# Performance work log

Measured on AMD Instinct MI355X. Metric: run time of the kernel, lower is better.

The kernel has to match this reference:

```python
import jax, jax.numpy as jnp
import numpy as np

B, C, H, W = 4096, 2, 64, 64
D = 1.0 / (H - 1)  # grid spacing d0 = d1
CLAMP_MIN = -27.6310211159


def fd1_last(f, d):
    # 2nd-order accurate first derivative along last axis, non-periodic.
    c = (f[..., 2:] - f[..., :-2]) / (2.0 * d)
    lo = (-3.0 * f[..., 0:1] + 4.0 * f[..., 1:2] - f[..., 2:3]) / (2.0 * d)
    hi = (3.0 * f[..., -1:] - 4.0 * f[..., -2:-1] + f[..., -3:-2]) / (2.0 * d)
    return jnp.concatenate([lo, c, hi], axis=-1)


def fd2_last(f, d):
    # 2nd-order accurate second derivative along last axis, non-periodic.
    d2 = d * d
    c = (f[..., 2:] - 2.0 * f[..., 1:-1] + f[..., :-2]) / d2
    lo = (2.0 * f[..., 0:1] - 5.0 * f[..., 1:2] + 4.0 * f[..., 2:3] - f[..., 3:4]) / d2
    hi = (2.0 * f[..., -1:] - 5.0 * f[..., -2:-1] + 4.0 * f[..., -3:-2] - f[..., -4:-3]) / d2
    return jnp.concatenate([lo, c, hi], axis=-1)


def fd_axis(f, d, axis, order):
    fn = fd1_last if order == 1 else fd2_last
    if axis == -1 or axis == f.ndim - 1:
        return fn(f, d)
    g = jnp.swapaxes(f, axis, -1)
    return jnp.swapaxes(fn(g, d), axis, -1)


def darcy_source(h, w, r=10.0, w_frac=0.125):
    ww = int(round(w_frac * h))
    f = np.zeros((h, w), dtype=np.float32)
    f[:ww, :ww] = r
    f[-ww:, -ww:] = -r
    return jnp.asarray(f)


def compute_residual(x0):
    # x0: (B, 2, H, W) with channel 0 = pressure p, channel 1 = permeability K
    p, perm = x0[:, 0], x0[:, 1]
    p_d0 = fd_axis(p, D, -2, 1)
    p_d1 = fd_axis(p, D, -1, 1)
    p_d00 = fd_axis(p, D, -2, 2)
    p_d11 = fd_axis(p, D, -1, 2)
    perm_d0 = fd_axis(perm, D, -2, 1)
    perm_d1 = fd_axis(perm, D, -1, 1)

    f_s = darcy_source(H, W)  # (H, W)
    # div(-K grad p) - f  (only diagonal of velocity jacobian is populated)
    eq0 = (-perm * p_d00 - perm_d0 * p_d0) + (-perm * p_d11 - perm_d1 * p_d1) - f_s  # (B,H,W)

    # Neumann boundary residuals on grad p (channel 0 = d/d0, channel 1 = d/d1)
    bc = jnp.zeros((x0.shape[0], 2, H, W), dtype=x0.dtype)
    bc = bc.at[:, 0, 0, :].set(-p_d0[:, 0, :])
    bc = bc.at[:, 0, -1, :].set(p_d0[:, -1, :])
    bc = bc.at[:, 1, :, 0].set(p_d1[:, :, 0])
    bc = bc.at[:, 1, :, -1].set(-p_d1[:, :, -1])

    # b c x y -> b (x y) c  layout, then concat eq0 as an extra channel
    eq0_flat = eq0.reshape(eq0.shape[0], H * W, 1)
    bc_flat = jnp.transpose(bc, (0, 2, 3, 1)).reshape(bc.shape[0], H * W, 2)
    residual = jnp.concatenate([eq0_flat, bc_flat], axis=-1)  # (B, HW, 3)
    return residual.mean(axis=(1, 2))  # (B,)


def darcy_loss(model_out, target, x0_hat, var):
    data_loss = jnp.mean((model_out - target) ** 2)
    r = compute_residual(x0_hat)  # (B,)
    ll = -0.5 * (r ** 2) / var  # gaussian log-likelihood of 0 under N(r, var)
    ll = jnp.maximum(ll, CLAMP_MIN)
    residual_loss = jnp.mean(-ll)
    c_residual = 1.0
    return data_loss + c_residual * residual_loss


def setup_inputs() -> dict:
    key = jax.random.key(0)
    k1, k2, k3, k4 = jax.random.split(key, 4)
    return {
        "model_out": jax.random.normal(k1, (B, C, H, W), dtype=jnp.float32),
        "target": jax.random.normal(k2, (B, C, H, W), dtype=jnp.float32),
        "x0_hat": jax.random.normal(k3, (B, C, H, W), dtype=jnp.float32),
        "var": jax.random.uniform(k4, (B,), dtype=jnp.float32, minval=0.5, maxval=1.5),
    }


def reference(model_out, target, x0_hat, var):
    return darcy_loss(model_out, target, x0_hat, var)
```

## Files before the change

kernel.cpp:

```cpp
#include <hip/hip_runtime.h>


#define NB 4096
#define HW 4096
#define CHW 8192

__device__ __forceinline__ void hderiv2(float v, int j, float& d1, float& d11) {
    constexpr float INV2D = 31.5f, INVD2 = 3969.0f;
    float vm = __shfl(v, (j + 63) & 63);
    float vp = __shfl(v, (j + 1) & 63);
    float v2 = __shfl(v, (j == 0) ? 2 : 61);
    float v3 = __shfl(v, (j == 0) ? 3 : 60);
    d1  = (vp - vm) * INV2D;
    d11 = (vp - 2.0f * v + vm) * INVD2;
    if (j == 0)  { d1 = (-3.0f * v + 4.0f * vp - v2) * INV2D;
                   d11 = (2.0f * v - 5.0f * vp + 4.0f * v2 - v3) * INVD2; }
    if (j == 63) { d1 = ( 3.0f * v - 4.0f * vm + v2) * INV2D;
                   d11 = (2.0f * v - 5.0f * vm + 4.0f * v2 - v3) * INVD2; }
}

__device__ __forceinline__ float hderiv1(float v, int j) {
    constexpr float INV2D = 31.5f;
    float vm = __shfl(v, (j + 63) & 63);
    float vp = __shfl(v, (j + 1) & 63);
    float v2 = __shfl(v, (j == 0) ? 2 : 61);
    float d = (vp - vm) * INV2D;
    if (j == 0)  d = (-3.0f * v + 4.0f * vp - v2) * INV2D;
    if (j == 63) d = ( 3.0f * v - 4.0f * vm + v2) * INV2D;
    return d;
}

__global__ __launch_bounds__(256, 8) void darcy_wave_kernel(
    const float* __restrict__ mo, const float* __restrict__ tg,
    const float* __restrict__ x0, const float* __restrict__ var,
    float* __restrict__ ws_res, float* __restrict__ ws_data)
{
    constexpr float INV2D = 31.5f;
    constexpr float INVD2 = 3969.0f;
    constexpr float CLAMP = 27.6310211159f;

    const int wave = threadIdx.x >> 6;
    const int j    = threadIdx.x & 63;
    const int b    = blockIdx.x * 4 + wave;

    const float*  pb = x0 + (size_t)b * CHW;
    const float*  qb = pb + HW;
    const float4* m4 = (const float4*)(mo + (size_t)b * CHW);
    const float4* g4 = (const float4*)(tg + (size_t)b * CHW);

    float rsum = 0.0f, dsum = 0.0f;

    float pm = pb[j], pc = pb[64 + j], pp = pb[128 + j], pn = pb[192 + j];
    float qm = qb[j], qc = qb[64 + j], qp = qb[128 + j], qn = qb[192 + j];

    {
        float pd1, pd11;
        hderiv2(pm, j, pd1, pd11);
        float qd1 = hderiv1(qm, j);
        float pd0  = (-3.0f * pm + 4.0f * pc - pp) * INV2D;
        float pd00 = (2.0f * pm - 5.0f * pc + 4.0f * pp - pn) * INVD2;
        float qd0  = (-3.0f * qm + 4.0f * qc - qp) * INV2D;
        rsum += -qm * (pd00 + pd11) - qd0 * pd0 - qd1 * pd1 - pd0;
        rsum += (j == 0) ? pd1 : 0.0f;
        rsum -= (j == 63) ? pd1 : 0.0f;
    }

    float s_p60 = 0.0f, s_p61 = 0.0f, s_q61 = 0.0f;

    #pragma unroll 2
    for (int i = 1; i <= 62; ++i) {
        float pn2 = 0.0f, qn2 = 0.0f;
        if (i <= 60) {
            pn2 = pb[((i + 3) << 6) + j];
            qn2 = qb[((i + 3) << 6) + j];
        }
        if (i <= 32) {
            const int k = (i - 1) << 6;
            float4 a = m4[j + k];
            float4 c = g4[j + k];
            float e0 = a.x - c.x, e1 = a.y - c.y, e2 = a.z - c.z, e3 = a.w - c.w;
            dsum += e0 * e0 + e1 * e1 + e2 * e2 + e3 * e3;
        }

        float pd1, pd11;
        hderiv2(pc, j, pd1, pd11);
        float qd1 = hderiv1(qc, j);
        float pd0  = (pp - pm) * INV2D;
        float pd00 = (pp - 2.0f * pc + pm) * INVD2;
        float qd0  = (qp - qm) * INV2D;
        rsum += -qc * (pd00 + pd11) - qd0 * pd0 - qd1 * pd1;
        rsum += (j == 0) ? pd1 : 0.0f;
        rsum -= (j == 63) ? pd1 : 0.0f;

        if (i == 61) s_p60 = pm;
        if (i == 62) { s_p61 = pm; s_q61 = qm; }

        pm = pc; pc = pp; pp = pn; pn = pn2;
        qm = qc; qc = qp; qp = qn; qn = qn2;
    }

    {
        float pd1, pd11;
        hderiv2(pc, j, pd1, pd11);
        float qd1 = hderiv1(qc, j);
        float pd0  = (3.0f * pc - 4.0f * pm + s_p61) * INV2D;
        float pd00 = (2.0f * pc - 5.0f * pm + 4.0f * s_p61 - s_p60) * INVD2;
        float qd0  = (3.0f * qc - 4.0f * qm + s_q61) * INV2D;
        rsum += -qc * (pd00 + pd11) - qd0 * pd0 - qd1 * pd1 + pd0;
        rsum += (j == 0) ? pd1 : 0.0f;
        rsum -= (j == 63) ? pd1 : 0.0f;
    }

    #pragma unroll
    for (int off = 32; off > 0; off >>= 1) {
        rsum += __shfl_down(rsum, off);
        dsum += __shfl_down(dsum, off);
    }
    if (j == 0) {
        const float r = rsum * (1.0f / (64.0f * 64.0f * 3.0f));
        float res = 0.5f * r * r / var[b];
        ws_res[b]  = fminf(res, CLAMP);
        ws_data[b] = dsum;
    }
}

__global__ __launch_bounds__(256) void darcy_final_kernel(
    const float* __restrict__ ws_res, const float* __restrict__ ws_data,
    float* __restrict__ out)
{
    const int t = threadIdx.x;
    double rs = 0.0, ds = 0.0;
    for (int i = t; i < NB; i += 256) {
        rs += (double)ws_res[i];
        ds += (double)ws_data[i];
    }
    #pragma unroll
    for (int off = 32; off > 0; off >>= 1) {
        rs += __shfl_down(rs, off);
        ds += __shfl_down(ds, off);
    }
    __shared__ double red[8];
    const int wid = t >> 6, lane = t & 63;
    if (lane == 0) { red[wid] = rs; red[4 + wid] = ds; }
    __syncthreads();
    if (t == 0) {
        const double R  = red[0] + red[1] + red[2] + red[3];
        const double Dd = red[4] + red[5] + red[6] + red[7];
        out[0] = (float)(Dd / ((double)NB * (double)CHW) + R / (double)NB);
    }
}

extern "C" void kernel_launch(void* const* d_in, const int* in_sizes, int n_in,
                              void* d_out, int out_size, void* d_ws, size_t ws_size,
                              hipStream_t stream) {
    const float* mo  = (const float*)d_in[0];
    const float* tg  = (const float*)d_in[1];
    const float* x0  = (const float*)d_in[2];
    const float* var = (const float*)d_in[3];
    float* out = (float*)d_out;

    float* ws_res  = (float*)d_ws;
    float* ws_data = ws_res + NB;

    darcy_wave_kernel<<<NB / 4, 256, 0, stream>>>(mo, tg, x0, var, ws_res, ws_data);
    darcy_final_kernel<<<1, 256, 0, stream>>>(ws_res, ws_data, out);
}
```

Measured before the change: 84.90 us.

## Split each batch row-sweep across two waves to double parallelism

Each batch element is now handled by two waves, one sweeping rows 0-31 and the other rows 32-63, with the data-loss float4 loads divided between them. Partial sums for each half go to the workspace, and the final kernel combines the halves before applying the variance scaling and clamp. The aim is more waves in flight and a shorter serial sweep per wave, which helps hide memory latency. The cost is some extra halo row loads, twice as many blocks, and a final kernel that reads twice the workspace plus the var array.

```diff
diff --git a/kernel.cpp b/kernel.cpp
--- a/kernel.cpp
+++ b/kernel.cpp
@@ -32,16 +32,15 @@
 
 __global__ __launch_bounds__(256, 8) void darcy_wave_kernel(
     const float* __restrict__ mo, const float* __restrict__ tg,
-    const float* __restrict__ x0, const float* __restrict__ var,
-    float* __restrict__ ws_res, float* __restrict__ ws_data)
+    const float* __restrict__ x0, float* __restrict__ ws_r, float* __restrict__ ws_d)
 {
     constexpr float INV2D = 31.5f;
     constexpr float INVD2 = 3969.0f;
-    constexpr float CLAMP = 27.6310211159f;
 
     const int wave = threadIdx.x >> 6;
     const int j    = threadIdx.x & 63;
-    const int b    = blockIdx.x * 4 + wave;
+    const int half = wave & 1;
+    const int b    = blockIdx.x * 2 + (wave >> 1);
 
     const float*  pb = x0 + (size_t)b * CHW;
     const float*  qb = pb + HW;
@@ -50,65 +49,103 @@
 
     float rsum = 0.0f, dsum = 0.0f;
 
-    float pm = pb[j], pc = pb[64 + j], pp = pb[128 + j], pn = pb[192 + j];
-    float qm = qb[j], qc = qb[64 + j], qp = qb[128 + j], qn = qb[192 + j];
-
-    {
-        float pd1, pd11;
-        hderiv2(pm, j, pd1, pd11);
-        float qd1 = hderiv1(qm, j);
-        float pd0  = (-3.0f * pm + 4.0f * pc - pp) * INV2D;
-        float pd00 = (2.0f * pm - 5.0f * pc + 4.0f * pp - pn) * INVD2;
-        float qd0  = (-3.0f * qm + 4.0f * qc - qp) * INV2D;
-        rsum += -qm * (pd00 + pd11) - qd0 * pd0 - qd1 * pd1 - pd0;
-        rsum += (j == 0) ? pd1 : 0.0f;
-        rsum -= (j == 63) ? pd1 : 0.0f;
-    }
-
-    float s_p60 = 0.0f, s_p61 = 0.0f, s_q61 = 0.0f;
-
-    #pragma unroll 2
-    for (int i = 1; i <= 62; ++i) {
-        float pn2 = 0.0f, qn2 = 0.0f;
-        if (i <= 60) {
-            pn2 = pb[((i + 3) << 6) + j];
-            qn2 = qb[((i + 3) << 6) + j];
-        }
-        if (i <= 32) {
-            const int k = (i - 1) << 6;
-            float4 a = m4[j + k];
-            float4 c = g4[j + k];
+    if (half == 0) {
+        float pm = pb[j], pc = pb[64 + j], pp = pb[128 + j], pn = pb[192 + j];
+        float qm = qb[j], qc = qb[64 + j], qp = qb[128 + j], qn = qb[192 + j];
+
+        {
+            float4 a = m4[j], c = g4[j];
             float e0 = a.x - c.x, e1 = a.y - c.y, e2 = a.z - c.z, e3 = a.w - c.w;
             dsum += e0 * e0 + e1 * e1 + e2 * e2 + e3 * e3;
-        }
-
-        float pd1, pd11;
-        hderiv2(pc, j, pd1, pd11);
-        float qd1 = hderiv1(qc, j);
-        float pd0  = (pp - pm) * INV2D;
-        float pd00 = (pp - 2.0f * pc + pm) * INVD2;
-        float qd0  = (qp - qm) * INV2D;
-        rsum += -qc * (pd00 + pd11) - qd0 * pd0 - qd1 * pd1;
-        rsum += (j == 0) ? pd1 : 0.0f;
-        rsum -= (j == 63) ? pd1 : 0.0f;
-
-        if (i == 61) s_p60 = pm;
-        if (i == 62) { s_p61 = pm; s_q61 = qm; }
-
-        pm = pc; pc = pp; pp = pn; pn = pn2;
-        qm = qc; qc = qp; qp = qn; qn = qn2;
-    }
-
-    {
-        float pd1, pd11;
-        hderiv2(pc, j, pd1, pd11);
-        float qd1 = hderiv1(qc, j);
-        float pd0  = (3.0f * pc - 4.0f * pm + s_p61) * INV2D;
-        float pd00 = (2.0f * pc - 5.0f * pm + 4.0f * s_p61 - s_p60) * INVD2;
-        float qd0  = (3.0f * qc - 4.0f * qm + s_q61) * INV2D;
-        rsum += -qc * (pd00 + pd11) - qd0 * pd0 - qd1 * pd1 + pd0;
-        rsum += (j == 0) ? pd1 : 0.0f;
-        rsum -= (j == 63) ? pd1 : 0.0f;
+
+            float pd1, pd11;
+            hderiv2(pm, j, pd1, pd11);
+            float qd1 = hderiv1(qm, j);
+            float pd0  = (-3.0f * pm + 4.0f * pc - pp) * INV2D;
+            float pd00 = (2.0f * pm - 5.0f * pc + 4.0f * pp - pn) * INVD2;
+            float qd0  = (-3.0f * qm + 4.0f * qc - qp) * INV2D;
+            rsum += -qm * (pd00 + pd11) - qd0 * pd0 - qd1 * pd1 - pd0;
+            rsum += (j == 0) ? pd1 : 0.0f;
+            rsum -= (j == 63) ? pd1 : 0.0f;
+        }
+
+        #pragma unroll 2
+        for (int i = 1; i <= 31; ++i) {
+            float pn2 = pb[((i + 3) << 6) + j];
+            float qn2 = qb[((i + 3) << 6) + j];
+            if (i & 1) {
+                const int c4 = (((i + 1) >> 1) << 6) + j;
+                float4 a = m4[c4], c = g4[c4];
+                float e0 = a.x - c.x, e1 = a.y - c.y, e2 = a.z - c.z, e3 = a.w - c.w;
+                dsum += e0 * e0 + e1 * e1 + e2 * e2 + e3 * e3;
+            }
+
+            float pd1, pd11;
+            hderiv2(pc, j, pd1, pd11);
+            float qd1 = hderiv1(qc, j);
+            float pd0  = (pp - pm) * INV2D;
+            float pd00 = (pp - 2.0f * pc + pm) * INVD2;
+            float qd0  = (qp - qm) * INV2D;
+            rsum += -qc * (pd00 + pd11) - qd0 * pd0 - qd1 * pd1;
+            rsum += (j == 0) ? pd1 : 0.0f;
+            rsum -= (j == 63) ? pd1 : 0.0f;
+
+            pm = pc; pc = pp; pp = pn; pn = pn2;
+            qm = qc; qc = qp; qp = qn; qn = qn2;
+        }
+    } else {
+        float pm = pb[31 * 64 + j], pc = pb[32 * 64 + j], pp = pb[33 * 64 + j], pn = pb[34 * 64 + j];
+        float qm = qb[31 * 64 + j], qc = qb[32 * 64 + j], qp = qb[33 * 64 + j], qn = qb[34 * 64 + j];
+
+        float s_p60 = 0.0f, s_p61 = 0.0f, s_q61 = 0.0f;
+
+        #pragma unroll 2
+        for (int i = 32; i <= 62; ++i) {
+            float pn2 = 0.0f, qn2 = 0.0f;
+            if (i <= 60) {
+                pn2 = pb[((i + 3) << 6) + j];
+                qn2 = qb[((i + 3) << 6) + j];
+            }
+            if (!(i & 1)) {
+                const int c4 = ((16 + ((i - 32) >> 1)) << 6) + j;
+                float4 a = m4[c4], c = g4[c4];
+                float e0 = a.x - c.x, e1 = a.y - c.y, e2 = a.z - c.z, e3 = a.w - c.w;
+                dsum += e0 * e0 + e1 * e1 + e2 * e2 + e3 * e3;
+            }
+
+            float pd1, pd11;
+            hderiv2(pc, j, pd1, pd11);
+            float qd1 = hderiv1(qc, j);
+            float pd0  = (pp - pm) * INV2D;
+            float pd00 = (pp - 2.0f * pc + pm) * INVD2;
+            float qd0  = (qp - qm) * INV2D;
+            rsum += -qc * (pd00 + pd11) - qd0 * pd0 - qd1 * pd1;
+            rsum += (j == 0) ? pd1 : 0.0f;
+            rsum -= (j == 63) ? pd1 : 0.0f;
+
+            if (i == 61) s_p60 = pm;
+            if (i == 62) { s_p61 = pm; s_q61 = qm; }
+
+            pm = pc; pc = pp; pp = pn; pn = pn2;
+            qm = qc; qc = qp; qp = qn; qn = qn2;
+        }
+
+        {
+            const int c4 = (31 << 6) + j;
+            float4 a = m4[c4], c = g4[c4];
+            float e0 = a.x - c.x, e1 = a.y - c.y, e2 = a.z - c.z, e3 = a.w - c.w;
+            dsum += e0 * e0 + e1 * e1 + e2 * e2 + e3 * e3;
+
+            float pd1, pd11;
+            hderiv2(pc, j, pd1, pd11);
+            float qd1 = hderiv1(qc, j);
+            float pd0  = (3.0f * pc - 4.0f * pm + s_p61) * INV2D;
+            float pd00 = (2.0f * pc - 5.0f * pm + 4.0f * s_p61 - s_p60) * INVD2;
+            float qd0  = (3.0f * qc - 4.0f * qm + s_q61) * INV2D;
+            rsum += -qc * (pd00 + pd11) - qd0 * pd0 - qd1 * pd1 + pd0;
+            rsum += (j == 0) ? pd1 : 0.0f;
+            rsum -= (j == 63) ? pd1 : 0.0f;
+        }
     }
 
     #pragma unroll
@@ -117,22 +154,24 @@
         dsum += __shfl_down(dsum, off);
     }
     if (j == 0) {
-        const float r = rsum * (1.0f / (64.0f * 64.0f * 3.0f));
-        float res = 0.5f * r * r / var[b];
-        ws_res[b]  = fminf(res, CLAMP);
-        ws_data[b] = dsum;
+        ws_r[half * NB + b] = rsum;
+        ws_d[half * NB + b] = dsum;
     }
 }
 
 __global__ __launch_bounds__(256) void darcy_final_kernel(
-    const float* __restrict__ ws_res, const float* __restrict__ ws_data,
-    float* __restrict__ out)
+    const float* __restrict__ ws_r, const float* __restrict__ ws_d,
+    const float* __restrict__ var, float* __restrict__ out)
 {
+    constexpr float CLAMP = 27.6310211159f;
     const int t = threadIdx.x;
     double rs = 0.0, ds = 0.0;
     for (int i = t; i < NB; i += 256) {
-        rs += (double)ws_res[i];
-        ds += (double)ws_data[i];
+        const float rb = ws_r[i] + ws_r[NB + i];
+        const float r  = rb * (1.0f / (64.0f * 64.0f * 3.0f));
+        float res = 0.5f * r * r / var[i];
+        rs += (double)fminf(res, CLAMP);
+        ds += (double)(ws_d[i] + ws_d[NB + i]);
     }
     #pragma unroll
     for (int off = 32; off > 0; off >>= 1) {
@@ -159,9 +198,9 @@
     const float* var = (const float*)d_in[3];
     float* out = (float*)d_out;
 
-    float* ws_res  = (float*)d_ws;
-    float* ws_data = ws_res + NB;
-
-    darcy_wave_kernel<<<NB / 4, 256, 0, stream>>>(mo, tg, x0, var, ws_res, ws_data);
-    darcy_final_kernel<<<1, 256, 0, stream>>>(ws_res, ws_data, out);
-}
+    float* ws_r = (float*)d_ws;
+    float* ws_d = ws_r + 2 * NB;
+
+    darcy_wave_kernel<<<NB / 2, 256, 0, stream>>>(mo, tg, x0, ws_r, ws_d);
+    darcy_final_kernel<<<1, 256, 0, stream>>>(ws_r, ws_d, var, out);
+}
```

Result: slower. 93.70 us (+10.4%).

## Split data-loss streaming into separate interleaved blocks with nontemporal grid-stride loads

Applied to the files above, without the earlier changes.

Moves the MSE data-loss reduction out of the per-batch stencil waves into dedicated even-numbered blocks. These blocks stream model_out and target with grid-strided nontemporal vector loads and write one partial per block. Odd blocks now run only the residual stencil. The aim is to balance memory traffic across blocks and stop the stencil loop from carrying the extra MSE loads, at the cost of twice as many blocks and a differently shaped final reduction.

```diff
diff --git a/kernel.cpp b/kernel.cpp
--- a/kernel.cpp
+++ b/kernel.cpp
@@ -4,6 +4,12 @@
 #define NB 4096
 #define HW 4096
 #define CHW 8192
+#define N4 8388608
+#define SBLOCKS 1024
+#define STRIDE (SBLOCKS * 256)
+#define PER_TH (N4 / STRIDE)
+
+typedef float vf4 __attribute__((ext_vector_type(4)));
 
 __device__ __forceinline__ void hderiv2(float v, int j, float& d1, float& d11) {
     constexpr float INV2D = 31.5f, INVD2 = 3969.0f;
@@ -30,25 +36,65 @@
     return d;
 }
 
-__global__ __launch_bounds__(256, 8) void darcy_wave_kernel(
+__global__ __launch_bounds__(256, 8) void darcy_main_kernel(
     const float* __restrict__ mo, const float* __restrict__ tg,
     const float* __restrict__ x0, const float* __restrict__ var,
-    float* __restrict__ ws_res, float* __restrict__ ws_data)
+    float* __restrict__ ws_res, float* __restrict__ ws_d)
 {
     constexpr float INV2D = 31.5f;
     constexpr float INVD2 = 3969.0f;
     constexpr float CLAMP = 27.6310211159f;
 
+    if ((blockIdx.x & 1) == 0) {
+        const int sb  = blockIdx.x >> 1;
+        const int tid = sb * 256 + threadIdx.x;
+        const vf4* m4 = (const vf4*)mo;
+        const vf4* g4 = (const vf4*)tg;
+
+        float acc0 = 0.0f, acc1 = 0.0f, acc2 = 0.0f, acc3 = 0.0f;
+        #pragma unroll
+        for (int k = 0; k < PER_TH; k += 4) {
+            const int i0 = tid + (k + 0) * STRIDE;
+            const int i1 = tid + (k + 1) * STRIDE;
+            const int i2 = tid + (k + 2) * STRIDE;
+            const int i3 = tid + (k + 3) * STRIDE;
+            vf4 a0 = __builtin_nontemporal_load(m4 + i0);
+            vf4 a1 = __builtin_nontemporal_load(m4 + i1);
+            vf4 a2 = __builtin_nontemporal_load(m4 + i2);
+            vf4 a3 = __builtin_nontemporal_load(m4 + i3);
+            vf4 c0 = __builtin_nontemporal_load(g4 + i0);
+            vf4 c1 = __builtin_nontemporal_load(g4 + i1);
+            vf4 c2 = __builtin_nontemporal_load(g4 + i2);
+            vf4 c3 = __builtin_nontemporal_load(g4 + i3);
+            vf4 d0 = a0 - c0, d1 = a1 - c1, d2 = a2 - c2, d3 = a3 - c3;
+            acc0 += d0.x * d0.x + d1.x * d1.x + d2.x * d2.x + d3.x * d3.x;
+            acc1 += d0.y * d0.y + d1.y * d1.y + d2.y * d2.y + d3.y * d3.y;
+            acc2 += d0.z * d0.z + d1.z * d1.z + d2.z * d2.z + d3.z * d3.z;
+            acc3 += d0.w * d0.w + d1.w * d1.w + d2.w * d2.w + d3.w * d3.w;
+        }
+        float dsum = (acc0 + acc1) + (acc2 + acc3);
+
+        #pragma unroll
+        for (int off = 32; off > 0; off >>= 1)
+            dsum += __shfl_down(dsum, off);
+
+        __shared__ float red[4];
+        const int wid = threadIdx.x >> 6, lane = threadIdx.x & 63;
+        if (lane == 0) red[wid] = dsum;
+        __syncthreads();
+        if (threadIdx.x == 0)
+            ws_d[sb] = red[0] + red[1] + red[2] + red[3];
+        return;
+    }
+
     const int wave = threadIdx.x >> 6;
     const int j    = threadIdx.x & 63;
-    const int b    = blockIdx.x * 4 + wave;
-
-    const float*  pb = x0 + (size_t)b * CHW;
-    const float*  qb = pb + HW;
-    const float4* m4 = (const float4*)(mo + (size_t)b * CHW);
-    const float4* g4 = (const float4*)(tg + (size_t)b * CHW);
-
-    float rsum = 0.0f, dsum = 0.0f;
+    const int b    = (blockIdx.x >> 1) * 4 + wave;
+
+    const float* pb = x0 + (size_t)b * CHW;
+    const float* qb = pb + HW;
+
+    float rsum = 0.0f;
 
     float pm = pb[j], pc = pb[64 + j], pp = pb[128 + j], pn = pb[192 + j];
     float qm = qb[j], qc = qb[64 + j], qp = qb[128 + j], qn = qb[192 + j];
@@ -74,13 +120,6 @@
             pn2 = pb[((i + 3) << 6) + j];
             qn2 = qb[((i + 3) << 6) + j];
         }
-        if (i <= 32) {
-            const int k = (i - 1) << 6;
-            float4 a = m4[j + k];
-            float4 c = g4[j + k];
-            float e0 = a.x - c.x, e1 = a.y - c.y, e2 = a.z - c.z, e3 = a.w - c.w;
-            dsum += e0 * e0 + e1 * e1 + e2 * e2 + e3 * e3;
-        }
 
         float pd1, pd11;
         hderiv2(pc, j, pd1, pd11);
@@ -112,28 +151,24 @@
     }
 
     #pragma unroll
-    for (int off = 32; off > 0; off >>= 1) {
+    for (int off = 32; off > 0; off >>= 1)
         rsum += __shfl_down(rsum, off);
-        dsum += __shfl_down(dsum, off);
-    }
+
     if (j == 0) {
         const float r = rsum * (1.0f / (64.0f * 64.0f * 3.0f));
         float res = 0.5f * r * r / var[b];
-        ws_res[b]  = fminf(res, CLAMP);
-        ws_data[b] = dsum;
+        ws_res[b] = fminf(res, CLAMP);
     }
 }
 
 __global__ __launch_bounds__(256) void darcy_final_kernel(
-    const float* __restrict__ ws_res, const float* __restrict__ ws_data,
+    const float* __restrict__ ws_res, const float* __restrict__ ws_d,
     float* __restrict__ out)
 {
     const int t = threadIdx.x;
     double rs = 0.0, ds = 0.0;
-    for (int i = t; i < NB; i += 256) {
-        rs += (double)ws_res[i];
-        ds += (double)ws_data[i];
-    }
+    for (int i = t; i < NB; i += 256) rs += (double)ws_res[i];
+    for (int i = t; i < SBLOCKS; i += 256) ds += (double)ws_d[i];
     #pragma unroll
     for (int off = 32; off > 0; off >>= 1) {
         rs += __shfl_down(rs, off);
@@ -159,9 +194,9 @@
     const float* var = (const float*)d_in[3];
     float* out = (float*)d_out;
 
-    float* ws_res  = (float*)d_ws;
-    float* ws_data = ws_res + NB;
-
-    darcy_wave_kernel<<<NB / 4, 256, 0, stream>>>(mo, tg, x0, var, ws_res, ws_data);
-    darcy_final_kernel<<<1, 256, 0, stream>>>(ws_res, ws_data, out);
-}
+    float* ws_res = (float*)d_ws;
+    float* ws_d   = ws_res + NB;
+
+    darcy_main_kernel<<<2 * SBLOCKS, 256, 0, stream>>>(mo, tg, x0, var, ws_res, ws_d);
+    darcy_final_kernel<<<1, 256, 0, stream>>>(ws_res, ws_d, out);
+}
```

Measured after the change: 83.84 us. About the same (-1.2%).

## Process four rows per wave step with float4 loads and cross-row shuffles

Applied to the files above, without the earlier changes.

Changes the per-wave layout so each lane holds four consecutive columns (a float4) and each 16-lane group covers one row. A wave now handles four rows per iteration, 16 iterations in total, and vertical neighbours are fetched with lane shuffles. It also switches the model_out/target loads to nontemporal loads and lowers the occupancy hint. The aim is fewer, wider memory instructions and fewer serial iterations, at the cost of more shuffles, boundary-select logic and register pressure.

```diff
diff --git a/kernel.cpp b/kernel.cpp
--- a/kernel.cpp
+++ b/kernel.cpp
@@ -5,110 +5,134 @@
 #define HW 4096
 #define CHW 8192
 
-__device__ __forceinline__ void hderiv2(float v, int j, float& d1, float& d11) {
-    constexpr float INV2D = 31.5f, INVD2 = 3969.0f;
-    float vm = __shfl(v, (j + 63) & 63);
-    float vp = __shfl(v, (j + 1) & 63);
-    float v2 = __shfl(v, (j == 0) ? 2 : 61);
-    float v3 = __shfl(v, (j == 0) ? 3 : 60);
-    d1  = (vp - vm) * INV2D;
-    d11 = (vp - 2.0f * v + vm) * INVD2;
-    if (j == 0)  { d1 = (-3.0f * v + 4.0f * vp - v2) * INV2D;
-                   d11 = (2.0f * v - 5.0f * vp + 4.0f * v2 - v3) * INVD2; }
-    if (j == 63) { d1 = ( 3.0f * v - 4.0f * vm + v2) * INV2D;
-                   d11 = (2.0f * v - 5.0f * vm + 4.0f * v2 - v3) * INVD2; }
+typedef float vf4 __attribute__((ext_vector_type(4)));
+
+__device__ __forceinline__ vf4 shfl4(vf4 v, int src) {
+    vf4 r;
+    r.x = __shfl(v.x, src); r.y = __shfl(v.y, src);
+    r.z = __shfl(v.z, src); r.w = __shfl(v.w, src);
+    return r;
+}
+__device__ __forceinline__ vf4 sel4(bool c, vf4 a, vf4 b) {
+    vf4 r;
+    r.x = c ? a.x : b.x; r.y = c ? a.y : b.y;
+    r.z = c ? a.z : b.z; r.w = c ? a.w : b.w;
+    return r;
 }
 
-__device__ __forceinline__ float hderiv1(float v, int j) {
-    constexpr float INV2D = 31.5f;
-    float vm = __shfl(v, (j + 63) & 63);
-    float vp = __shfl(v, (j + 1) & 63);
-    float v2 = __shfl(v, (j == 0) ? 2 : 61);
-    float d = (vp - vm) * INV2D;
-    if (j == 0)  d = (-3.0f * v + 4.0f * vp - v2) * INV2D;
-    if (j == 63) d = ( 3.0f * v - 4.0f * vm + v2) * INV2D;
-    return d;
-}
-
-__global__ __launch_bounds__(256, 8) void darcy_wave_kernel(
+__global__ __launch_bounds__(256, 4) void darcy_fused_kernel(
     const float* __restrict__ mo, const float* __restrict__ tg,
     const float* __restrict__ x0, const float* __restrict__ var,
-    float* __restrict__ ws_res, float* __restrict__ ws_data)
+    float* __restrict__ ws_res, float* __restrict__ ws_d)
 {
     constexpr float INV2D = 31.5f;
     constexpr float INVD2 = 3969.0f;
     constexpr float CLAMP = 27.6310211159f;
 
-    const int wave = threadIdx.x >> 6;
-    const int j    = threadIdx.x & 63;
-    const int b    = blockIdx.x * 4 + wave;
+    const int lane = threadIdx.x & 63;
+    const int wv   = threadIdx.x >> 6;
+    const int b    = blockIdx.x * 4 + wv;
+    const int g    = lane >> 4;
+    const bool g0  = (g == 0), g3 = (g == 3);
+    const bool cL  = ((lane & 15) == 0);
+    const bool cR  = ((lane & 15) == 15);
 
-    const float*  pb = x0 + (size_t)b * CHW;
-    const float*  qb = pb + HW;
-    const float4* m4 = (const float4*)(mo + (size_t)b * CHW);
-    const float4* g4 = (const float4*)(tg + (size_t)b * CHW);
+    const vf4* p4 = (const vf4*)(x0 + (size_t)b * CHW);
+    const vf4* q4 = p4 + 1024;
+    const vf4* m4 = (const vf4*)(mo + (size_t)b * CHW);
+    const vf4* g4 = (const vf4*)(tg + (size_t)b * CHW);
+
+    const int iu = (lane + 16) & 63;
+    const int id = (lane + 48) & 63;
+    const int ix = (lane + 32) & 63;
+    const int il = (lane + 63) & 63;
+    const int ir = (lane + 1) & 63;
 
     float rsum = 0.0f, dsum = 0.0f;
 
-    float pm = pb[j], pc = pb[64 + j], pp = pb[128 + j], pn = pb[192 + j];
-    float qm = qb[j], qc = qb[64 + j], qp = qb[128 + j], qn = qb[192 + j];
+    vf4 pc = p4[lane], qc = q4[lane];
+    vf4 pv = pc, qv = qc;
 
-    {
-        float pd1, pd11;
-        hderiv2(pm, j, pd1, pd11);
-        float qd1 = hderiv1(qm, j);
-        float pd0  = (-3.0f * pm + 4.0f * pc - pp) * INV2D;
-        float pd00 = (2.0f * pm - 5.0f * pc + 4.0f * pp - pn) * INVD2;
-        float qd0  = (-3.0f * qm + 4.0f * qc - qp) * INV2D;
-        rsum += -qm * (pd00 + pd11) - qd0 * pd0 - qd1 * pd1 - pd0;
-        rsum += (j == 0) ? pd1 : 0.0f;
-        rsum -= (j == 63) ? pd1 : 0.0f;
-    }
+    #pragma unroll 4
+    for (int t = 0; t < 16; ++t) {
+        vf4 pn_, qn_;
+        if (t < 15) { pn_ = p4[(t + 1) * 64 + lane]; qn_ = q4[(t + 1) * 64 + lane]; }
+        else        { pn_ = pc; qn_ = qc; }
 
-    float s_p60 = 0.0f, s_p61 = 0.0f, s_q61 = 0.0f;
+        vf4 a0 = __builtin_nontemporal_load(m4 + t * 128 + lane);
+        vf4 a1 = __builtin_nontemporal_load(m4 + t * 128 + 64 + lane);
+        vf4 e0 = a0 - __builtin_nontemporal_load(g4 + t * 128 + lane);
+        vf4 e1 = a1 - __builtin_nontemporal_load(g4 + t * 128 + 64 + lane);
+        dsum += e0.x*e0.x + e0.y*e0.y + e0.z*e0.z + e0.w*e0.w
+              + e1.x*e1.x + e1.y*e1.y + e1.z*e1.z + e1.w*e1.w;
 
-    #pragma unroll 2
-    for (int i = 1; i <= 62; ++i) {
-        float pn2 = 0.0f, qn2 = 0.0f;
-        if (i <= 60) {
-            pn2 = pb[((i + 3) << 6) + j];
-            qn2 = qb[((i + 3) << 6) + j];
+        vf4 upc = shfl4(pc, iu), dnc = shfl4(pc, id);
+        vf4 upq = shfl4(qc, iu), dnq = shfl4(qc, id);
+        vf4 upn = shfl4(pn_, iu), dnp = shfl4(pv, id);
+        vf4 uqn = shfl4(qn_, iu), dqp = shfl4(qv, id);
+        vf4 upP = sel4(g3, upn, upc);
+        vf4 dnP = sel4(g0, dnp, dnc);
+        vf4 upQ = sel4(g3, uqn, upq);
+        vf4 dnQ = sel4(g0, dqp, dnq);
+
+        vf4 pd0  = (upP - dnP) * INV2D;
+        vf4 pd00 = (upP - 2.0f * pc + dnP) * INVD2;
+        vf4 qd0  = (upQ - dnQ) * INV2D;
+
+        if (t == 0) {
+            vf4 r2 = shfl4(pc, ix);
+            vf4 s2 = shfl4(qc, ix);
+            vf4 od0  = (-3.0f * pc + 4.0f * upc - r2) * INV2D;
+            vf4 od00 = (2.0f * pc - 5.0f * upc + 4.0f * r2 - dnc) * INVD2;
+            vf4 oq0  = (-3.0f * qc + 4.0f * upq - s2) * INV2D;
+            pd0  = sel4(g0, od0, pd0);
+            pd00 = sel4(g0, od00, pd00);
+            qd0  = sel4(g0, oq0, qd0);
         }
-        if (i <= 32) {
-            const int k = (i - 1) << 6;
-            float4 a = m4[j + k];
-            float4 c = g4[j + k];
-            float e0 = a.x - c.x, e1 = a.y - c.y, e2 = a.z - c.z, e3 = a.w - c.w;
-            dsum += e0 * e0 + e1 * e1 + e2 * e2 + e3 * e3;
+        if (t == 15) {
+            vf4 m2 = shfl4(pc, ix);
+            vf4 s2 = shfl4(qc, ix);
+            vf4 od0  = (3.0f * pc - 4.0f * dnc + m2) * INV2D;
+            vf4 od00 = (2.0f * pc - 5.0f * dnc + 4.0f * m2 - upc) * INVD2;
+            vf4 oq0  = (3.0f * qc - 4.0f * dnq + s2) * INV2D;
+            pd0  = sel4(g3, od0, pd0);
+            pd00 = sel4(g3, od00, pd00);
+            qd0  = sel4(g3, oq0, qd0);
         }
 
-        float pd1, pd11;
-        hderiv2(pc, j, pd1, pd11);
-        float qd1 = hderiv1(qc, j);
-        float pd0  = (pp - pm) * INV2D;
-        float pd00 = (pp - 2.0f * pc + pm) * INVD2;
-        float qd0  = (qp - qm) * INV2D;
-        rsum += -qc * (pd00 + pd11) - qd0 * pd0 - qd1 * pd1;
-        rsum += (j == 0) ? pd1 : 0.0f;
-        rsum -= (j == 63) ? pd1 : 0.0f;
+        float pL = __shfl(pc.w, il), pR = __shfl(pc.x, ir);
+        float qL = __shfl(qc.w, il), qR = __shfl(qc.x, ir);
 
-        if (i == 61) s_p60 = pm;
-        if (i == 62) { s_p61 = pm; s_q61 = qm; }
+        float pd1_0  = cL ? (-3.f*pc.x + 4.f*pc.y - pc.z) * INV2D
+                          : (pc.y - pL) * INV2D;
+        float pd11_0 = cL ? (2.f*pc.x - 5.f*pc.y + 4.f*pc.z - pc.w) * INVD2
+                          : (pc.y - 2.f*pc.x + pL) * INVD2;
+        float qd1_0  = cL ? (-3.f*qc.x + 4.f*qc.y - qc.z) * INV2D
+                          : (qc.y - qL) * INV2D;
+        float pd1_1  = (pc.z - pc.x) * INV2D;
+        float pd11_1 = (pc.z - 2.f*pc.y + pc.x) * INVD2;
+        float qd1_1  = (qc.z - qc.x) * INV2D;
+        float pd1_2  = (pc.w - pc.y) * INV2D;
+        float pd11_2 = (pc.w - 2.f*pc.z + pc.y) * INVD2;
+        float qd1_2  = (qc.w - qc.y) * INV2D;
+        float pd1_3  = cR ? (3.f*pc.w - 4.f*pc.z + pc.y) * INV2D
+                          : (pR - pc.z) * INV2D;
+        float pd11_3 = cR ? (2.f*pc.w - 5.f*pc.z + 4.f*pc.y - pc.x) * INVD2
+                          : (pR - 2.f*pc.w + pc.z) * INVD2;
+        float qd1_3  = cR ? (3.f*qc.w - 4.f*qc.z + qc.y) * INV2D
+                          : (qR - qc.z) * INV2D;
 
-        pm = pc; pc = pp; pp = pn; pn = pn2;
-        qm = qc; qc = qp; qp = qn; qn = qn2;
-    }
+        rsum -= qc.x * (pd00.x + pd11_0) + qd0.x * pd0.x + qd1_0 * pd1_0;
+        rsum -= qc.y * (pd00.y + pd11_1) + qd0.y * pd0.y + qd1_1 * pd1_1;
+        rsum -= qc.z * (pd00.z + pd11_2) + qd0.z * pd0.z + qd1_2 * pd1_2;
+        rsum -= qc.w * (pd00.w + pd11_3) + qd0.w * pd0.w + qd1_3 * pd1_3;
 
-    {
-        float pd1, pd11;
-        hderiv2(pc, j, pd1, pd11);
-        float qd1 = hderiv1(qc, j);
-        float pd0  = (3.0f * pc - 4.0f * pm + s_p61) * INV2D;
-        float pd00 = (2.0f * pc - 5.0f * pm + 4.0f * s_p61 - s_p60) * INVD2;
-        float qd0  = (3.0f * qc - 4.0f * qm + s_q61) * INV2D;
-        rsum += -qc * (pd00 + pd11) - qd0 * pd0 - qd1 * pd1 + pd0;
-        rsum += (j == 0) ? pd1 : 0.0f;
-        rsum -= (j == 63) ? pd1 : 0.0f;
+        if (t == 0)  rsum -= g0 ? (pd0.x + pd0.y + pd0.z + pd0.w) : 0.0f;
+        if (t == 15) rsum += g3 ? (pd0.x + pd0.y + pd0.z + pd0.w) : 0.0f;
+        rsum += cL ? pd1_0 : 0.0f;
+        rsum -= cR ? pd1_3 : 0.0f;
+
+        pv = pc; qv = qc; pc = pn_; qc = qn_;
     }
 
     #pragma unroll
@@ -116,23 +140,23 @@
         rsum += __shfl_down(rsum, off);
         dsum += __shfl_down(dsum, off);
     }
-    if (j == 0) {
+    if (lane == 0) {
         const float r = rsum * (1.0f / (64.0f * 64.0f * 3.0f));
         float res = 0.5f * r * r / var[b];
-        ws_res[b]  = fminf(res, CLAMP);
-        ws_data[b] = dsum;
+        ws_res[b] = fminf(res, CLAMP);
+        ws_d[b]   = dsum;
     }
 }
 
 __global__ __launch_bounds__(256) void darcy_final_kernel(
-    const float* __restrict__ ws_res, const float* __restrict__ ws_data,
+    const float* __restrict__ ws_res, const float* __restrict__ ws_d,
     float* __restrict__ out)
 {
     const int t = threadIdx.x;
     double rs = 0.0, ds = 0.0;
     for (int i = t; i < NB; i += 256) {
         rs += (double)ws_res[i];
-        ds += (double)ws_data[i];
+        ds += (double)ws_d[i];
     }
     #pragma unroll
     for (int off = 32; off > 0; off >>= 1) {
@@ -159,9 +183,9 @@
     const float* var = (const float*)d_in[3];
     float* out = (float*)d_out;
 
-    float* ws_res  = (float*)d_ws;
-    float* ws_data = ws_res + NB;
+    float* ws_res = (float*)d_ws;
+    float* ws_d   = ws_res + NB;
 
-    darcy_wave_kernel<<<NB / 4, 256, 0, stream>>>(mo, tg, x0, var, ws_res, ws_data);
-    darcy_final_kernel<<<1, 256, 0, stream>>>(ws_res, ws_data, out);
+    darcy_fused_kernel<<<NB / 4, 256, 0, stream>>>(mo, tg, x0, var, ws_res, ws_d);
+    darcy_final_kernel<<<1, 256, 0, stream>>>(ws_res, ws_d, out);
 }
```

Result: slower. 264.4 us (+211.4%).
